# Kernel tuning notes

Measured on AMD Instinct MI355X. Metric: run time of the kernel, lower is better.

The kernel has to match this reference:

```python
import jax, jax.numpy as jnp
import numpy as np

EPS = 1e-8


def setup_inputs() -> dict:
    key = jax.random.key(0)
    k1, k2 = jax.random.split(key)
    a = jax.random.normal(k1, (1, 256, 128, 128), dtype=jnp.float32)
    b = jax.random.normal(k2, (1, 256, 128, 128), dtype=jnp.float32)
    return {"a": a, "b": b}


def reference(a, b):
    # a: [n, c, h, w] rendered feats; b: [n, c, h2, w2] style feats (n == 1)
    n, c, h, w = a.shape
    a_flat = a.reshape(n, c, -1)            # [n, c, hw]
    b_flat = b.reshape(n, c, -1)            # [n, c, h2w2]

    # argmin_cos_distance: channel-wise L2 normalize, cosine distance, argmin
    b_norm = jnp.sqrt((b_flat * b_flat).sum(1, keepdims=True) + EPS)
    b_n = b_flat / (b_norm + EPS)
    a_norm = jnp.sqrt((a_flat * a_flat).sum(1, keepdims=True) + EPS)
    a_n = a_flat / (a_norm + EPS)
    d_mat = 1.0 - jnp.einsum('ncp,ncq->npq', a_n, b_n)   # [n, hw, h2w2]
    z_best = jnp.argmin(d_mat, axis=2)                    # [n, hw]

    # nn_feat_replace: gather matched (unnormalized) style features
    idx = jnp.broadcast_to(z_best[:, None, :], b_flat.shape)
    target = jnp.take_along_axis(b_flat, idx, axis=2).reshape(n, c, h, w)

    # cos_loss(a, target): cosine distance over channel dim, mean over pixels
    an = jnp.sqrt((a * a).sum(1, keepdims=True))
    tn = jnp.sqrt((target * target).sum(1, keepdims=True))
    cossim = ((a / (an + EPS)) * (target / (tn + EPS))).sum(1)  # [n, h, w]
    return (1.0 - cossim).mean()
```

## Files before the change

kernel.cpp:

```cpp
#include <hip/hip_runtime.h>
#include <hip/hip_fp8.h>
#include <stdint.h>

#define EPS 1e-8f

constexpr int C  = 256;
constexpr int HW = 16384;
constexpr int BM = 128;
constexpr int NG = 2048;

typedef __attribute__((ext_vector_type(4))) float floatx4;
typedef long long llong2 __attribute__((ext_vector_type(2)));
typedef unsigned char u8;
typedef unsigned int u32;
typedef unsigned long long u64;

__device__ inline u8 f2fp8(float x) {
    __hip_fp8_e4m3 h(x);
    return h.__x;
}

__global__ __launch_bounds__(256) void prep_kernel(const float* __restrict__ a,
                                                   const float* __restrict__ b,
                                                   float* __restrict__ sumsq_a,
                                                   float* __restrict__ sumsq_b,
                                                   u8* __restrict__ aF, u8* __restrict__ bF) {
    __shared__ float red[16][65];
    __shared__ float invb_sh[64];
    const int tid = threadIdx.x;
    const int pg = tid & 15, tc = tid >> 4;
    const int p0 = blockIdx.x * 64, pb = pg * 4;

    float4 bv[16];
    float ss0 = 0.f, ss1 = 0.f, ss2 = 0.f, ss3 = 0.f;
    #pragma unroll
    for (int i = 0; i < 16; ++i) {
        bv[i] = *(const float4*)&b[(size_t)(tc * 16 + i) * HW + p0 + pb];
        ss0 += bv[i].x * bv[i].x; ss1 += bv[i].y * bv[i].y;
        ss2 += bv[i].z * bv[i].z; ss3 += bv[i].w * bv[i].w;
    }
    red[tc][pb] = ss0; red[tc][pb + 1] = ss1; red[tc][pb + 2] = ss2; red[tc][pb + 3] = ss3;
    __syncthreads();
    if (tid < 64) {
        float B = 0.f;
        #pragma unroll
        for (int j = 0; j < 16; ++j) B += red[j][tid];
        sumsq_b[p0 + tid] = B;
        invb_sh[tid] = 1.0f / (sqrtf(B + EPS) + EPS);
    }
    __syncthreads();

    #pragma unroll
    for (int j = 0; j < 4; ++j) {
        int p = p0 + pb + j;
        float inv = invb_sh[pb + j];
        int g = p >> 4;
        #pragma unroll
        for (int h = 0; h < 2; ++h) {
            int cb = tc * 2 + h;
            u64 wv = 0;
            #pragma unroll
            for (int k = 0; k < 8; ++k) {
                const float4& f = bv[h * 8 + k];
                float v = (j == 0) ? f.x : (j == 1) ? f.y : (j == 2) ? f.z : f.w;
                wv |= (u64)f2fp8(v * inv) << (8 * k);
            }
            int lane2 = (p & 15) + ((cb & 3) << 4);
            *(u64*)(bF + (((size_t)(g * 4 + (cb >> 3))) << 10) + lane2 * 16 + ((cb >> 2) & 1) * 8) = wv;
        }
    }

    float4 av[16];
    ss0 = ss1 = ss2 = ss3 = 0.f;
    #pragma unroll
    for (int i = 0; i < 16; ++i) {
        av[i] = *(const float4*)&a[(size_t)(tc * 16 + i) * HW + p0 + pb];
        ss0 += av[i].x * av[i].x; ss1 += av[i].y * av[i].y;
        ss2 += av[i].z * av[i].z; ss3 += av[i].w * av[i].w;
    }
    #pragma unroll
    for (int j = 0; j < 4; ++j) {
        int p = p0 + pb + j;
        int g = p >> 4;
        #pragma unroll
        for (int h = 0; h < 2; ++h) {
            int cb = tc * 2 + h;
            u64 wv = 0;
            #pragma unroll
            for (int k = 0; k < 8; ++k) {
                const float4& f = av[h * 8 + k];
                float v = (j == 0) ? f.x : (j == 1) ? f.y : (j == 2) ? f.z : f.w;
                wv |= (u64)f2fp8(v) << (8 * k);
            }
            int lane2 = (p & 15) + ((cb & 3) << 4);
            *(u64*)(aF + (((size_t)(g * 4 + (cb >> 3))) << 10) + lane2 * 16 + ((cb >> 2) & 1) * 8) = wv;
        }
    }
    red[tc][pb] = ss0; red[tc][pb + 1] = ss1; red[tc][pb + 2] = ss2; red[tc][pb + 3] = ss3;
    __syncthreads();
    if (tid < 64) {
        float A = 0.f;
        #pragma unroll
        for (int j = 0; j < 16; ++j) A += red[j][tid];
        sumsq_a[p0 + tid] = A;
    }
}

__global__ __launch_bounds__(256, 3) void gemm_argmax(const u8* __restrict__ aF,
                                                      const u8* __restrict__ bF,
                                                      u64* __restrict__ packed) {
    const int tid = threadIdx.x;
    const int w = tid >> 6, lane = tid & 63;
    const int q4 = lane >> 4, r15 = lane & 15;
    const int wm = w >> 1, wn = w & 1;

    const u32 bid = blockIdx.x;
    const u32 ng = bid & 7;
    const u32 mt = bid >> 3;
    const int p0 = (int)mt * BM;

    const u8* gA = aF + ((size_t)(mt * 8 + wm * 4) * 4) * 1024 + (u32)lane * 16;
    llong2 Afr[4][4];
    #pragma unroll
    for (int mi = 0; mi < 4; ++mi)
        #pragma unroll
        for (int cp = 0; cp < 4; ++cp)
            Afr[mi][cp] = *(const llong2*)(gA + (u32)(mi * 4 + cp) * 1024);

    const u8* gB = bF + ((size_t)(ng * 128 + wn * 2)) * 4096 + (u32)lane * 16;

    float bestv[4][4];
    u32   bestq[4][4];
    #pragma unroll
    for (int mi = 0; mi < 4; ++mi)
        #pragma unroll
        for (int reg = 0; reg < 4; ++reg) { bestv[mi][reg] = -3.4e38f; bestq[mi][reg] = 0; }

    const u32 qlane = ng * 2048 + wn * 32 + (u32)r15;

    llong2 Bfr[2][2];
    #pragma unroll
    for (int ni = 0; ni < 2; ++ni)
        Bfr[0][ni] = *(const llong2*)(gB + (u32)ni * 4096u);

    for (int qt = 0; qt < 32; ++qt) {
        floatx4 acc[4][2] = {};
        #pragma unroll
        for (int cp = 0; cp < 4; ++cp) {
            const int cur = cp & 1, nxt = cur ^ 1;
            u32 nqt = (cp == 3) ? (u32)(qt + 1 < 32 ? qt + 1 : 31) : (u32)qt;
            u32 ncp = (cp == 3) ? 0u : (u32)(cp + 1);
            #pragma unroll
            for (int ni = 0; ni < 2; ++ni)
                Bfr[nxt][ni] = *(const llong2*)(gB + nqt * 16384u + (u32)ni * 4096u + ncp * 1024u);
            #pragma unroll
            for (int mi = 0; mi < 4; ++mi)
                #pragma unroll
                for (int ni = 0; ni < 2; ++ni)
                    acc[mi][ni] = __builtin_amdgcn_mfma_f32_16x16x32_fp8_fp8(
                        Afr[mi][cp].x, Bfr[cur][ni].x, acc[mi][ni], 0, 0, 0);
            #pragma unroll
            for (int mi = 0; mi < 4; ++mi)
                #pragma unroll
                for (int ni = 0; ni < 2; ++ni)
                    acc[mi][ni] = __builtin_amdgcn_mfma_f32_16x16x32_fp8_fp8(
                        Afr[mi][cp].y, Bfr[cur][ni].y, acc[mi][ni], 0, 0, 0);
        }
        #pragma unroll
        for (int mi = 0; mi < 4; ++mi)
            #pragma unroll
            for (int ni = 0; ni < 2; ++ni) {
                u32 qc = qlane + (u32)qt * 64 + (u32)ni * 16;
                #pragma unroll
                for (int reg = 0; reg < 4; ++reg) {
                    float v = acc[mi][ni][reg];
                    bool gt = v > bestv[mi][reg];
                    bestv[mi][reg] = gt ? v : bestv[mi][reg];
                    bestq[mi][reg] = gt ? qc : bestq[mi][reg];
                }
            }
    }

    #pragma unroll
    for (int mi = 0; mi < 4; ++mi)
        #pragma unroll
        for (int reg = 0; reg < 4; ++reg) {
            u32 m = __float_as_uint(bestv[mi][reg]);
            m = m ^ (u32)(((int)m >> 31) | 0x80000000u);
            u64 pk = ((u64)m << 32) | (u64)(0xFFFFFFFFu - bestq[mi][reg]);
            #pragma unroll
            for (int d = 1; d < 16; d <<= 1) {
                u64 o = __shfl_xor((unsigned long long)pk, d);
                pk = o > pk ? o : pk;
            }
            if (r15 == 0)
                atomicMax(&packed[p0 + wm * 64 + mi * 16 + q4 * 4 + reg], pk);
        }
}

__global__ void loss_kernel(const u64* __restrict__ packed,
                            const float* __restrict__ sumsq_a, const float* __restrict__ sumsq_b,
                            float* __restrict__ out) {
    int p = blockIdx.x * 256 + threadIdx.x;
    u64 pk = packed[p];
    u32 m = (u32)(pk >> 32);
    u32 u = (m & 0x80000000u) ? (m ^ 0x80000000u) : ~m;
    float s = __uint_as_float(u);
    u32 q = 0xFFFFFFFFu - (u32)(pk & 0xFFFFFFFFull);
    float A = sumsq_a[p], B = sumsq_b[q];
    float dot = s * (sqrtf(B + EPS) + EPS);
    float cossim = dot / ((sqrtf(A) + EPS) * (sqrtf(B) + EPS));
    float v = (1.0f - cossim) * (1.0f / (float)HW);
    #pragma unroll
    for (int d = 1; d < 64; d <<= 1) v += __shfl_xor(v, d);
    if ((threadIdx.x & 63) == 0) atomicAdd(out, v);
}

extern "C" void kernel_launch(void* const* d_in, const int* in_sizes, int n_in,
                              void* d_out, int out_size, void* d_ws, size_t ws_size,
                              hipStream_t stream) {
    const float* a = (const float*)d_in[0];
    const float* b = (const float*)d_in[1];
    float* out = (float*)d_out;
    char* ws = (char*)d_ws;

    u8*    aF      = (u8*)ws;
    u8*    bF      = (u8*)(ws + (size_t)4 * 1024 * 1024);
    float* sumsq_a = (float*)(ws + (size_t)8 * 1024 * 1024);
    float* sumsq_b = sumsq_a + HW;
    u64*   packed  = (u64*)(sumsq_b + HW);

    hipMemsetAsync(out, 0, sizeof(float), stream);
    hipMemsetAsync(packed, 0, (size_t)HW * sizeof(u64), stream);

    prep_kernel<<<dim3(HW / 64), 256, 0, stream>>>(a, b, sumsq_a, sumsq_b, aF, bF);
    gemm_argmax<<<dim3((HW / BM) * (HW / NG)), 256, 0, stream>>>(aF, bF, packed);
    loss_kernel<<<dim3(HW / 256), 256, 0, stream>>>(packed, sumsq_a, sumsq_b, out);
}
```

Measured before the change: 170.0 us.

## Switch to 16x16x128 scaled FP8 MFMA with fp64-packed argmax and new fragment layout

Replaces the 16x16x32 fp8 MFMA loop with the gfx950 scaled 16x16x128 f8f6f4 MFMA, cutting the MFMA instruction count per tile by 4x. The prep kernel now writes a matching 32-byte-per-lane fragment layout using packed hardware fp8 conversions. Argmax tracking is folded into a single fmax on a double: a +64 bias keeps scores positive so the float bits and inverted index pack into a monotonic 64-bit value. The bias is subtracted again in the loss kernel. Occupancy hint drops from 3 to 2 waves per SIMD because the larger fragments use more registers.

```diff
diff --git a/kernel.cpp b/kernel.cpp
--- a/kernel.cpp
+++ b/kernel.cpp
@@ -1,23 +1,26 @@
 #include <hip/hip_runtime.h>
-#include <hip/hip_fp8.h>
 #include <stdint.h>
 
 #define EPS 1e-8f
 
-constexpr int C  = 256;
 constexpr int HW = 16384;
 constexpr int BM = 128;
 constexpr int NG = 2048;
 
 typedef __attribute__((ext_vector_type(4))) float floatx4;
-typedef long long llong2 __attribute__((ext_vector_type(2)));
+typedef __attribute__((ext_vector_type(8))) int   intx8;
 typedef unsigned char u8;
 typedef unsigned int u32;
 typedef unsigned long long u64;
 
-__device__ inline u8 f2fp8(float x) {
-    __hip_fp8_e4m3 h(x);
-    return h.__x;
+__device__ inline u32 pk4(float x0, float x1, float x2, float x3) {
+    int t = __builtin_amdgcn_cvt_pk_fp8_f32(x0, x1, 0, false);
+    t = __builtin_amdgcn_cvt_pk_fp8_f32(x2, x3, t, true);
+    return (u32)t;
+}
+
+__device__ inline float getc(const float4& f, int j) {
+    return (j == 0) ? f.x : (j == 1) ? f.y : (j == 2) ? f.z : f.w;
 }
 
 __global__ __launch_bounds__(256) void prep_kernel(const float* __restrict__ a,
@@ -30,6 +33,7 @@
     const int tid = threadIdx.x;
     const int pg = tid & 15, tc = tid >> 4;
     const int p0 = blockIdx.x * 64, pb = pg * 4;
+    const int kb = tc >> 3, qg = (tc >> 1) & 3, lo16 = (tc & 1) * 16;
 
     float4 bv[16];
     float ss0 = 0.f, ss1 = 0.f, ss2 = 0.f, ss3 = 0.f;
@@ -52,22 +56,15 @@
 
     #pragma unroll
     for (int j = 0; j < 4; ++j) {
-        int p = p0 + pb + j;
-        float inv = invb_sh[pb + j];
-        int g = p >> 4;
-        #pragma unroll
-        for (int h = 0; h < 2; ++h) {
-            int cb = tc * 2 + h;
-            u64 wv = 0;
-            #pragma unroll
-            for (int k = 0; k < 8; ++k) {
-                const float4& f = bv[h * 8 + k];
-                float v = (j == 0) ? f.x : (j == 1) ? f.y : (j == 2) ? f.z : f.w;
-                wv |= (u64)f2fp8(v * inv) << (8 * k);
-            }
-            int lane2 = (p & 15) + ((cb & 3) << 4);
-            *(u64*)(bF + (((size_t)(g * 4 + (cb >> 3))) << 10) + lane2 * 16 + ((cb >> 2) & 1) * 8) = wv;
-        }
+        const int p = p0 + pb + j;
+        const int g = p >> 4, rp = (pb + j) & 15;
+        const float inv = invb_sh[pb + j];
+        int4 W;
+        W.x = (int)pk4(getc(bv[0], j) * inv, getc(bv[1], j) * inv, getc(bv[2], j) * inv, getc(bv[3], j) * inv);
+        W.y = (int)pk4(getc(bv[4], j) * inv, getc(bv[5], j) * inv, getc(bv[6], j) * inv, getc(bv[7], j) * inv);
+        W.z = (int)pk4(getc(bv[8], j) * inv, getc(bv[9], j) * inv, getc(bv[10], j) * inv, getc(bv[11], j) * inv);
+        W.w = (int)pk4(getc(bv[12], j) * inv, getc(bv[13], j) * inv, getc(bv[14], j) * inv, getc(bv[15], j) * inv);
+        *(int4*)(bF + (((size_t)(g * 2 + kb)) << 11) + (qg * 16 + rp) * 32 + lo16) = W;
     }
 
     float4 av[16];
@@ -80,21 +77,14 @@
     }
     #pragma unroll
     for (int j = 0; j < 4; ++j) {
-        int p = p0 + pb + j;
-        int g = p >> 4;
-        #pragma unroll
-        for (int h = 0; h < 2; ++h) {
-            int cb = tc * 2 + h;
-            u64 wv = 0;
-            #pragma unroll
-            for (int k = 0; k < 8; ++k) {
-                const float4& f = av[h * 8 + k];
-                float v = (j == 0) ? f.x : (j == 1) ? f.y : (j == 2) ? f.z : f.w;
-                wv |= (u64)f2fp8(v) << (8 * k);
-            }
-            int lane2 = (p & 15) + ((cb & 3) << 4);
-            *(u64*)(aF + (((size_t)(g * 4 + (cb >> 3))) << 10) + lane2 * 16 + ((cb >> 2) & 1) * 8) = wv;
-        }
+        const int p = p0 + pb + j;
+        const int g = p >> 4, rp = (pb + j) & 15;
+        int4 W;
+        W.x = (int)pk4(getc(av[0], j), getc(av[1], j), getc(av[2], j), getc(av[3], j));
+        W.y = (int)pk4(getc(av[4], j), getc(av[5], j), getc(av[6], j), getc(av[7], j));
+        W.z = (int)pk4(getc(av[8], j), getc(av[9], j), getc(av[10], j), getc(av[11], j));
+        W.w = (int)pk4(getc(av[12], j), getc(av[13], j), getc(av[14], j), getc(av[15], j));
+        *(int4*)(aF + (((size_t)(g * 2 + kb)) << 11) + (qg * 16 + rp) * 32 + lo16) = W;
     }
     red[tc][pb] = ss0; red[tc][pb + 1] = ss1; red[tc][pb + 2] = ss2; red[tc][pb + 3] = ss3;
     __syncthreads();
@@ -106,7 +96,7 @@
     }
 }
 
-__global__ __launch_bounds__(256, 3) void gemm_argmax(const u8* __restrict__ aF,
+__global__ __launch_bounds__(256, 2) void gemm_argmax(const u8* __restrict__ aF,
                                                       const u8* __restrict__ bF,
                                                       u64* __restrict__ packed) {
     const int tid = threadIdx.x;
@@ -119,64 +109,64 @@
     const u32 mt = bid >> 3;
     const int p0 = (int)mt * BM;
 
-    const u8* gA = aF + ((size_t)(mt * 8 + wm * 4) * 4) * 1024 + (u32)lane * 16;
-    llong2 Afr[4][4];
+    const u8* gA = aF + (((size_t)(mt * 8 + wm * 4)) << 12) + (u32)lane * 32;
+    intx8 Afr[4][2];
     #pragma unroll
     for (int mi = 0; mi < 4; ++mi)
         #pragma unroll
-        for (int cp = 0; cp < 4; ++cp)
-            Afr[mi][cp] = *(const llong2*)(gA + (u32)(mi * 4 + cp) * 1024);
-
-    const u8* gB = bF + ((size_t)(ng * 128 + wn * 2)) * 4096 + (u32)lane * 16;
-
-    float bestv[4][4];
-    u32   bestq[4][4];
+        for (int kb = 0; kb < 2; ++kb)
+            Afr[mi][kb] = *(const intx8*)(gA + (u32)(mi * 2 + kb) * 2048u);
+
+    const u8* gB = bF + (((size_t)(ng * 128 + wn * 2)) << 12) + (u32)lane * 32;
+
+    double best[4][4];
     #pragma unroll
     for (int mi = 0; mi < 4; ++mi)
         #pragma unroll
-        for (int reg = 0; reg < 4; ++reg) { bestv[mi][reg] = -3.4e38f; bestq[mi][reg] = 0; }
+        for (int r = 0; r < 4; ++r) best[mi][r] = 0.0;
 
     const u32 qlane = ng * 2048 + wn * 32 + (u32)r15;
-
-    llong2 Bfr[2][2];
+    const floatx4 C64 = {64.f, 64.f, 64.f, 64.f};
+    const int SCL = 0x7F7F7F7F;
+
+    intx8 Bfr[2][2];
     #pragma unroll
     for (int ni = 0; ni < 2; ++ni)
-        Bfr[0][ni] = *(const llong2*)(gB + (u32)ni * 4096u);
+        Bfr[0][ni] = *(const intx8*)(gB + (u32)ni * 4096u);
 
     for (int qt = 0; qt < 32; ++qt) {
-        floatx4 acc[4][2] = {};
-        #pragma unroll
-        for (int cp = 0; cp < 4; ++cp) {
-            const int cur = cp & 1, nxt = cur ^ 1;
-            u32 nqt = (cp == 3) ? (u32)(qt + 1 < 32 ? qt + 1 : 31) : (u32)qt;
-            u32 ncp = (cp == 3) ? 0u : (u32)(cp + 1);
+        const u32 qo = (u32)qt * 16384u;
+        floatx4 acc[4][2];
+        #pragma unroll
+        for (int ni = 0; ni < 2; ++ni)
+            Bfr[1][ni] = *(const intx8*)(gB + qo + (u32)ni * 4096u + 2048u);
+        #pragma unroll
+        for (int mi = 0; mi < 4; ++mi)
             #pragma unroll
             for (int ni = 0; ni < 2; ++ni)
-                Bfr[nxt][ni] = *(const llong2*)(gB + nqt * 16384u + (u32)ni * 4096u + ncp * 1024u);
-            #pragma unroll
-            for (int mi = 0; mi < 4; ++mi)
+                acc[mi][ni] = __builtin_amdgcn_mfma_scale_f32_16x16x128_f8f6f4(
+                    Afr[mi][0], Bfr[0][ni], C64, 0, 0, 0, SCL, 0, SCL);
+        const u32 nqo = (qt + 1 < 32) ? qo + 16384u : qo;
+        #pragma unroll
+        for (int ni = 0; ni < 2; ++ni)
+            Bfr[0][ni] = *(const intx8*)(gB + nqo + (u32)ni * 4096u);
+        #pragma unroll
+        for (int mi = 0; mi < 4; ++mi)
+            #pragma unroll
+            for (int ni = 0; ni < 2; ++ni)
+                acc[mi][ni] = __builtin_amdgcn_mfma_scale_f32_16x16x128_f8f6f4(
+                    Afr[mi][1], Bfr[1][ni], acc[mi][ni], 0, 0, 0, SCL, 0, SCL);
+
+        const u32 lo0 = 0xFFFFFFFFu - (qlane + (u32)qt * 64u);
+        #pragma unroll
+        for (int mi = 0; mi < 4; ++mi)
+            #pragma unroll
+            for (int ni = 0; ni < 2; ++ni) {
+                const u32 lw = lo0 - (u32)(ni * 16);
                 #pragma unroll
-                for (int ni = 0; ni < 2; ++ni)
-                    acc[mi][ni] = __builtin_amdgcn_mfma_f32_16x16x32_fp8_fp8(
-                        Afr[mi][cp].x, Bfr[cur][ni].x, acc[mi][ni], 0, 0, 0);
-            #pragma unroll
-            for (int mi = 0; mi < 4; ++mi)
-                #pragma unroll
-                for (int ni = 0; ni < 2; ++ni)
-                    acc[mi][ni] = __builtin_amdgcn_mfma_f32_16x16x32_fp8_fp8(
-                        Afr[mi][cp].y, Bfr[cur][ni].y, acc[mi][ni], 0, 0, 0);
-        }
-        #pragma unroll
-        for (int mi = 0; mi < 4; ++mi)
-            #pragma unroll
-            for (int ni = 0; ni < 2; ++ni) {
-                u32 qc = qlane + (u32)qt * 64 + (u32)ni * 16;
-                #pragma unroll
-                for (int reg = 0; reg < 4; ++reg) {
-                    float v = acc[mi][ni][reg];
-                    bool gt = v > bestv[mi][reg];
-                    bestv[mi][reg] = gt ? v : bestv[mi][reg];
-                    bestq[mi][reg] = gt ? qc : bestq[mi][reg];
+                for (int r = 0; r < 4; ++r) {
+                    u64 pk = ((u64)__float_as_uint(acc[mi][ni][r]) << 32) | (u64)lw;
+                    best[mi][r] = fmax(best[mi][r], __longlong_as_double((long long)pk));
                 }
             }
     }
@@ -184,17 +174,15 @@
     #pragma unroll
     for (int mi = 0; mi < 4; ++mi)
         #pragma unroll
-        for (int reg = 0; reg < 4; ++reg) {
-            u32 m = __float_as_uint(bestv[mi][reg]);
-            m = m ^ (u32)(((int)m >> 31) | 0x80000000u);
-            u64 pk = ((u64)m << 32) | (u64)(0xFFFFFFFFu - bestq[mi][reg]);
+        for (int r = 0; r < 4; ++r) {
+            u64 pk = (u64)__double_as_longlong(best[mi][r]);
             #pragma unroll
             for (int d = 1; d < 16; d <<= 1) {
                 u64 o = __shfl_xor((unsigned long long)pk, d);
                 pk = o > pk ? o : pk;
             }
             if (r15 == 0)
-                atomicMax(&packed[p0 + wm * 64 + mi * 16 + q4 * 4 + reg], pk);
+                atomicMax(&packed[p0 + wm * 64 + mi * 16 + q4 * 4 + r], pk);
         }
 }
 
@@ -203,9 +191,7 @@
                             float* __restrict__ out) {
     int p = blockIdx.x * 256 + threadIdx.x;
     u64 pk = packed[p];
-    u32 m = (u32)(pk >> 32);
-    u32 u = (m & 0x80000000u) ? (m ^ 0x80000000u) : ~m;
-    float s = __uint_as_float(u);
+    float s = __uint_as_float((u32)(pk >> 32)) - 64.0f;
     u32 q = 0xFFFFFFFFu - (u32)(pk & 0xFFFFFFFFull);
     float A = sumsq_a[p], B = sumsq_b[q];
     float dot = s * (sqrtf(B + EPS) + EPS);
```

Result: faster. 163.0 us (-4.1%).
